# Performance work log

Hardware: AMD Instinct MI355X
Metric: run time of the kernel (lower is better)

The kernel has to match this reference:

```python
import jax, jax.numpy as jnp
import numpy as np

BN_EPS = 1e-05
K3 = 27  # 3x3x3 octree kernel


def setup_inputs() -> dict:
    key = jax.random.key(0)
    k1, k2, k3 = jax.random.split(key, 3)
    C_in, C_out, H = 64, 128, 65536
    data_in = jax.random.normal(k1, (1, C_in, H, 1), dtype=jnp.float32)
    neigh = jax.random.randint(k2, (H, K3), 0, H, dtype=jnp.int32)
    weight = jax.random.normal(k3, (C_out, C_in, K3), dtype=jnp.float32) * 0.05
    gamma = jnp.ones((C_out,), dtype=jnp.float32)
    beta = jnp.zeros((C_out,), dtype=jnp.float32)
    return {"data_in": data_in, "neigh": neigh, "weight": weight,
            "gamma": gamma, "beta": beta}


def reference(data_in, neigh, weight, gamma, beta):
    # data_in: [1, C_in, H, 1] (ocnn octree feature layout)
    x = data_in[0, :, :, 0]                      # [C_in, H]
    col = x[:, neigh]                            # octree2col gather -> [C_in, H, K3]
    out = jnp.einsum('cnk,ock->on', col, weight)  # GEMM -> [C_out, H]
    # BatchNorm2d (training mode): stats over the node dim, per channel
    mean = jnp.mean(out, axis=1, keepdims=True)
    var = jnp.mean(jnp.square(out - mean), axis=1, keepdims=True)  # biased var
    y = (out - mean) * jax.lax.rsqrt(var + BN_EPS) * gamma[:, None] + beta[:, None]
    y = jnp.maximum(y, 0.0)                      # ReLU
    return y[None, :, :, None]                   # [1, C_out, H, 1]
```

## Files before the change

kernel.cpp:

```cpp
#include <hip/hip_runtime.h>

#define H 65536
#define CIN 64
#define COUT 128
#define NK 27
#define KTOT (NK*CIN)
#define NBLK 256
#define NTHR 1024
#define NBLOCKS (H/NBLK)

typedef unsigned short u16;
typedef unsigned int   u32;
typedef __attribute__((ext_vector_type(8))) short short8;
typedef __attribute__((ext_vector_type(4))) float f32x4;
typedef __attribute__((ext_vector_type(4))) unsigned int u32x4;

__device__ __forceinline__ u16 f2bf(float f) {
    u32 u = __float_as_uint(f);
    u = (u + 0x7FFFu + ((u >> 16) & 1u)) >> 16;
    return (u16)u;
}

__global__ __launch_bounds__(256) void transpose_x(const float* __restrict__ x,
                                                   u16* __restrict__ xt) {
    const int h = blockIdx.x * 256 + threadIdx.x;
    u32 pk[32];
#pragma unroll
    for (int cp = 0; cp < 32; ++cp) {
        float f0 = x[(2 * cp)     * H + h];
        float f1 = x[(2 * cp + 1) * H + h];
        pk[cp] = (u32)f2bf(f0) | ((u32)f2bf(f1) << 16);
    }
    u32x4* dst = (u32x4*)(xt + (size_t)h * CIN);
#pragma unroll
    for (int i = 0; i < 8; ++i)
        dst[i] = *(u32x4*)&pk[i * 4];
}

__global__ __launch_bounds__(256) void conv_w(const float* __restrict__ w,
                                              u16* __restrict__ wb,
                                              float* __restrict__ sums) {
    const int tid = blockIdx.x * 256 + threadIdx.x;
    if (blockIdx.x == 0) sums[threadIdx.x] = 0.f;
    if (tid < COUT * KTOT) {
        const int o = tid / KTOT;
        const int rem = tid - o * KTOT;
        const int k = rem >> 6;
        const int c = rem & 63;
        wb[tid] = f2bf(w[o * KTOT + c * NK + k]);
    }
}

__global__ __launch_bounds__(NTHR, 4) void conv_mfma(const u16* __restrict__ xt,
                                                     const u16* __restrict__ wb,
                                                     const int* __restrict__ neigh,
                                                     float* __restrict__ out,
                                                     float* __restrict__ part) {
    __shared__ __align__(16) u16 sB[3][NBLK * CIN];
    __shared__ u16 sIdx[NBLK * NK];

    const int tid  = threadIdx.x;
    const int lane = tid & 63;
    const int w    = tid >> 6;
    const int wo   = w >> 1;
    const int wn   = w & 1;
    const int n0   = blockIdx.x * NBLK;

    for (int i = tid; i < NBLK * NK; i += NTHR)
        sIdx[i] = (u16)neigh[n0 * NK + i];
    __syncthreads();

    const int r16 = lane & 15;
    const int q   = lane >> 4;
    const int kc  = q * 8;
    const int pl  = lane >> 3;
    const int cl  = lane & 7;

    f32x4 acc[8] = {};

    u32x4  rg[2][2];
    short8 af[2][2];

#define GATHER(K)                                                            \
    { _Pragma("unroll") for (int it = 0; it < 2; ++it) {                     \
        const int p_ = w * 16 + it * 8 + pl;                                 \
        const int row_ = sIdx[p_ * NK + (K)];                                \
        rg[(K) & 1][it] =                                                    \
            *(const u32x4*)(xt + (size_t)(u32)row_ * 64 + cl * 8); } }
#define WRITEB(K)                                                            \
    { _Pragma("unroll") for (int it = 0; it < 2; ++it) {                     \
        const int p_ = w * 16 + it * 8 + pl;                                 \
        *(u32x4*)(&sB[(K) % 3][p_ * 64 + ((cl ^ pl) * 8)]) = rg[(K) & 1][it]; } }
#define A_LOAD(K)                                                            \
    { _Pragma("unroll") for (int hh = 0; hh < 2; ++hh) {                     \
        const int o_ = wo * 16 + r16;                                        \
        af[(K) & 1][hh] = *(const short8*)(wb + (size_t)o_ * KTOT +          \
                                           (K) * CIN + hh * 32 + kc); } }
#define MFMA_STEP(K)                                                         \
    { _Pragma("unroll") for (int hh = 0; hh < 2; ++hh)                       \
      _Pragma("unroll") for (int g2 = 0; g2 < 2; ++g2) {                     \
        short8 bfr[4];                                                       \
        _Pragma("unroll") for (int j = 0; j < 4; ++j) {                      \
            const int nf = g2 * 4 + j;                                       \
            const int p_ = wn * 128 + nf * 16 + r16;                         \
            const int sl_ = (hh * 4 + q) ^ (p_ & 7);                         \
            bfr[j] = *(const short8*)(&sB[(K) % 3][p_ * 64 + sl_ * 8]);      \
        }                                                                    \
        _Pragma("unroll") for (int j = 0; j < 4; ++j)                        \
            acc[g2 * 4 + j] = __builtin_amdgcn_mfma_f32_16x16x32_bf16(       \
                af[(K) & 1][hh], bfr[j], acc[g2 * 4 + j], 0, 0, 0);          \
    } }

    GATHER(0)
    GATHER(1)
    WRITEB(0)
    WRITEB(1)
    A_LOAD(0)
    GATHER(2)
    GATHER(3)
    asm volatile("s_waitcnt lgkmcnt(0)" ::: "memory");

#pragma unroll
    for (int k = 0; k < NK; ++k) {
        __builtin_amdgcn_s_barrier();
        if (k + 2 < NK) WRITEB(k + 2)
        if (k + 1 < NK) A_LOAD(k + 1)
        if (k + 4 < NK) GATHER(k + 4)
        MFMA_STEP(k)
        asm volatile("s_waitcnt lgkmcnt(0)" ::: "memory");
    }

#undef GATHER
#undef WRITEB
#undef A_LOAD
#undef MFMA_STEP

#pragma unroll
    for (int nf = 0; nf < 8; ++nf)
#pragma unroll
        for (int r = 0; r < 4; ++r) {
            const int o = wo * 16 + q * 4 + r;
            const int n = n0 + wn * 128 + nf * 16 + r16;
            out[(size_t)o * H + n] = acc[nf][r];
        }

    float* red = (float*)sIdx;
    __syncthreads();
#pragma unroll
    for (int r = 0; r < 4; ++r) {
        float sv = 0.f, sq = 0.f;
#pragma unroll
        for (int nf = 0; nf < 8; ++nf) {
            sv += acc[nf][r];
            sq += acc[nf][r] * acc[nf][r];
        }
#pragma unroll
        for (int m = 1; m < 16; m <<= 1) {
            sv += __shfl_xor(sv, m, 64);
            sq += __shfl_xor(sq, m, 64);
        }
        if (r16 == 0) {
            const int o = wo * 16 + q * 4 + r;
            red[wn * 256 + o]       = sv;
            red[wn * 256 + 128 + o] = sq;
        }
    }
    __syncthreads();
    if (tid < 128) {
        part[(size_t)blockIdx.x * 256 + tid]       = red[tid] + red[256 + tid];
        part[(size_t)blockIdx.x * 256 + 128 + tid] = red[128 + tid] + red[384 + tid];
    }
}

__global__ __launch_bounds__(256) void bn_reduce(const float* __restrict__ part,
                                                 float* __restrict__ sums) {
    const int tid = threadIdx.x;
    float s = 0.f;
    const int b0 = blockIdx.x * (NBLOCKS / 16);
    for (int b = b0; b < b0 + NBLOCKS / 16; ++b)
        s += part[(size_t)b * 256 + tid];
    atomicAdd(&sums[tid], s);
}

__global__ __launch_bounds__(256) void bn_relu(float* __restrict__ out,
                                               const float* __restrict__ sums,
                                               const float* __restrict__ gamma,
                                               const float* __restrict__ beta) {
    const int idx = blockIdx.x * 256 + threadIdx.x;
    const int o = idx >> 14;
    const float mean = sums[o] * (1.f / (float)H);
    const float var  = sums[COUT + o] * (1.f / (float)H) - mean * mean;
    const float a = gamma[o] * rsqrtf(var + 1e-5f);
    const float b = beta[o] - mean * a;
    float4* p = (float4*)out;
    float4 v = p[idx];
    v.x = fmaxf(fmaf(v.x, a, b), 0.f);
    v.y = fmaxf(fmaf(v.y, a, b), 0.f);
    v.z = fmaxf(fmaf(v.z, a, b), 0.f);
    v.w = fmaxf(fmaf(v.w, a, b), 0.f);
    p[idx] = v;
}

extern "C" void kernel_launch(void* const* d_in, const int* in_sizes, int n_in,
                              void* d_out, int out_size, void* d_ws, size_t ws_size,
                              hipStream_t stream) {
    const float* x     = (const float*)d_in[0];
    const int*   neigh = (const int*)d_in[1];
    const float* w     = (const float*)d_in[2];
    const float* gamma = (const float*)d_in[3];
    const float* beta  = (const float*)d_in[4];
    float* out = (float*)d_out;

    char* ws = (char*)d_ws;
    u16* xt  = (u16*)ws;
    u16* wb  = (u16*)(ws + 8388608);
    float* sums = (float*)(ws + 8830976);
    float* part = (float*)(ws + 8832000);

    transpose_x<<<H / 256, 256, 0, stream>>>(x, xt);
    conv_w<<<(COUT * KTOT + 255) / 256, 256, 0, stream>>>(w, wb, sums);
    conv_mfma<<<NBLOCKS, NTHR, 0, stream>>>(xt, wb, neigh, out, part);
    bn_reduce<<<16, 256, 0, stream>>>(part, sums);
    bn_relu<<<(COUT * H / 4) / 256, 256, 0, stream>>>(out, sums, gamma, beta);
}
```

Baseline: 71.97 us.

## Store pre-BN conv output as bf16 intermediate and merge prep kernels

The conv kernel now writes its pre-normalization output as bf16 to a workspace buffer instead of fp32 to the final output. The BN+ReLU kernel reads that buffer, widens it to fp32 and writes the final result, so intermediate traffic is halved. The transpose and weight-conversion kernels are also merged into one launch to save a kernel launch. BN statistics still come from the fp32 accumulators, but the normalized values pick up bf16 rounding error, and the conv output stores are now 2-byte scattered writes.

```diff
diff --git a/kernel.cpp b/kernel.cpp
--- a/kernel.cpp
+++ b/kernel.cpp
@@ -12,6 +12,7 @@
 typedef unsigned short u16;
 typedef unsigned int   u32;
 typedef __attribute__((ext_vector_type(8))) short short8;
+typedef __attribute__((ext_vector_type(8))) unsigned short ushort8;
 typedef __attribute__((ext_vector_type(4))) float f32x4;
 typedef __attribute__((ext_vector_type(4))) unsigned int u32x4;
 
@@ -20,41 +21,47 @@
     u = (u + 0x7FFFu + ((u >> 16) & 1u)) >> 16;
     return (u16)u;
 }
-
-__global__ __launch_bounds__(256) void transpose_x(const float* __restrict__ x,
-                                                   u16* __restrict__ xt) {
-    const int h = blockIdx.x * 256 + threadIdx.x;
-    u32 pk[32];
-#pragma unroll
-    for (int cp = 0; cp < 32; ++cp) {
-        float f0 = x[(2 * cp)     * H + h];
-        float f1 = x[(2 * cp + 1) * H + h];
-        pk[cp] = (u32)f2bf(f0) | ((u32)f2bf(f1) << 16);
-    }
-    u32x4* dst = (u32x4*)(xt + (size_t)h * CIN);
-#pragma unroll
-    for (int i = 0; i < 8; ++i)
-        dst[i] = *(u32x4*)&pk[i * 4];
-}
-
-__global__ __launch_bounds__(256) void conv_w(const float* __restrict__ w,
-                                              u16* __restrict__ wb,
-                                              float* __restrict__ sums) {
-    const int tid = blockIdx.x * 256 + threadIdx.x;
-    if (blockIdx.x == 0) sums[threadIdx.x] = 0.f;
-    if (tid < COUT * KTOT) {
-        const int o = tid / KTOT;
-        const int rem = tid - o * KTOT;
-        const int k = rem >> 6;
-        const int c = rem & 63;
-        wb[tid] = f2bf(w[o * KTOT + c * NK + k]);
+__device__ __forceinline__ float bf2f(u16 v) {
+    u32 u = (u32)v << 16;
+    return __uint_as_float(u);
+}
+
+__global__ __launch_bounds__(256) void prep(const float* __restrict__ x,
+                                            const float* __restrict__ w,
+                                            u16* __restrict__ xt,
+                                            u16* __restrict__ wb,
+                                            float* __restrict__ sums) {
+    const int b = blockIdx.x;
+    if (b < 256) {
+        const int h = b * 256 + threadIdx.x;
+        u32 pk[32];
+#pragma unroll
+        for (int cp = 0; cp < 32; ++cp) {
+            float f0 = x[(2 * cp)     * H + h];
+            float f1 = x[(2 * cp + 1) * H + h];
+            pk[cp] = (u32)f2bf(f0) | ((u32)f2bf(f1) << 16);
+        }
+        u32x4* dst = (u32x4*)(xt + (size_t)h * CIN);
+#pragma unroll
+        for (int i = 0; i < 8; ++i)
+            dst[i] = *(u32x4*)&pk[i * 4];
+    } else {
+        if (b == 256) sums[threadIdx.x] = 0.f;
+        const int tid = (b - 256) * 256 + threadIdx.x;
+        if (tid < COUT * KTOT) {
+            const int o = tid / KTOT;
+            const int rem = tid - o * KTOT;
+            const int k = rem >> 6;
+            const int c = rem & 63;
+            wb[tid] = f2bf(w[o * KTOT + c * NK + k]);
+        }
     }
 }
 
 __global__ __launch_bounds__(NTHR, 4) void conv_mfma(const u16* __restrict__ xt,
                                                      const u16* __restrict__ wb,
                                                      const int* __restrict__ neigh,
-                                                     float* __restrict__ out,
+                                                     u16* __restrict__ obuf,
                                                      float* __restrict__ part) {
     __shared__ __align__(16) u16 sB[3][NBLK * CIN];
     __shared__ u16 sIdx[NBLK * NK];
@@ -141,7 +148,7 @@
         for (int r = 0; r < 4; ++r) {
             const int o = wo * 16 + q * 4 + r;
             const int n = n0 + wn * 128 + nf * 16 + r16;
-            out[(size_t)o * H + n] = acc[nf][r];
+            obuf[(size_t)o * H + n] = f2bf(acc[nf][r]);
         }
 
     float* red = (float*)sIdx;
@@ -182,23 +189,35 @@
     atomicAdd(&sums[tid], s);
 }
 
-__global__ __launch_bounds__(256) void bn_relu(float* __restrict__ out,
+__global__ __launch_bounds__(256) void bn_relu(const u16* __restrict__ obuf,
                                                const float* __restrict__ sums,
                                                const float* __restrict__ gamma,
-                                               const float* __restrict__ beta) {
-    const int idx = blockIdx.x * 256 + threadIdx.x;
-    const int o = idx >> 14;
+                                               const float* __restrict__ beta,
+                                               float* __restrict__ out) {
+    const int o     = blockIdx.x >> 4;
+    const int chunk = blockIdx.x & 15;
     const float mean = sums[o] * (1.f / (float)H);
     const float var  = sums[COUT + o] * (1.f / (float)H) - mean * mean;
     const float a = gamma[o] * rsqrtf(var + 1e-5f);
     const float b = beta[o] - mean * a;
-    float4* p = (float4*)out;
-    float4 v = p[idx];
-    v.x = fmaxf(fmaf(v.x, a, b), 0.f);
-    v.y = fmaxf(fmaf(v.y, a, b), 0.f);
-    v.z = fmaxf(fmaf(v.z, a, b), 0.f);
-    v.w = fmaxf(fmaf(v.w, a, b), 0.f);
-    p[idx] = v;
+    const size_t base = (size_t)o * H + chunk * 4096 + threadIdx.x * 16;
+    const ushort8* src = (const ushort8*)(obuf + base);
+    float4* dst = (float4*)(out + base);
+#pragma unroll
+    for (int v = 0; v < 2; ++v) {
+        ushort8 u = src[v];
+        float4 f0, f1;
+        f0.x = fmaxf(fmaf(bf2f(u[0]), a, b), 0.f);
+        f0.y = fmaxf(fmaf(bf2f(u[1]), a, b), 0.f);
+        f0.z = fmaxf(fmaf(bf2f(u[2]), a, b), 0.f);
+        f0.w = fmaxf(fmaf(bf2f(u[3]), a, b), 0.f);
+        f1.x = fmaxf(fmaf(bf2f(u[4]), a, b), 0.f);
+        f1.y = fmaxf(fmaf(bf2f(u[5]), a, b), 0.f);
+        f1.z = fmaxf(fmaf(bf2f(u[6]), a, b), 0.f);
+        f1.w = fmaxf(fmaf(bf2f(u[7]), a, b), 0.f);
+        dst[v * 2]     = f0;
+        dst[v * 2 + 1] = f1;
+    }
 }
 
 extern "C" void kernel_launch(void* const* d_in, const int* in_sizes, int n_in,
@@ -216,10 +235,10 @@
     u16* wb  = (u16*)(ws + 8388608);
     float* sums = (float*)(ws + 8830976);
     float* part = (float*)(ws + 8832000);
-
-    transpose_x<<<H / 256, 256, 0, stream>>>(x, xt);
-    conv_w<<<(COUT * KTOT + 255) / 256, 256, 0, stream>>>(w, wb, sums);
-    conv_mfma<<<NBLOCKS, NTHR, 0, stream>>>(xt, wb, neigh, out, part);
+    u16* obuf = (u16*)(ws + 9094144);
+
+    prep<<<1120, 256, 0, stream>>>(x, w, xt, wb, sums);
+    conv_mfma<<<NBLOCKS, NTHR, 0, stream>>>(xt, wb, neigh, obuf, part);
     bn_reduce<<<16, 256, 0, stream>>>(part, sums);
-    bn_relu<<<(COUT * H / 4) / 256, 256, 0, stream>>>(out, sums, gamma, beta);
-}
+    bn_relu<<<COUT * 16, 256, 0, stream>>>(obuf, sums, gamma, beta, out);
+}
```

Result: slower. 76.06 us (+5.7%).
